# Kernel tuning notes

Measured on AMD Instinct MI355X. Metric: run time of the kernel, lower is better.

## Reference

```python
import jax, jax.numpy as jnp
import numpy as np

GROUPS = 8
EPS = 1e-3  # Keras GroupNormalization default epsilon


def group_norm(x, gamma, beta):
    b, h, w, c = x.shape
    xr = x.reshape(b, h, w, GROUPS, c // GROUPS)
    mean = jnp.mean(xr, axis=(1, 2, 4), keepdims=True)
    var = jnp.var(xr, axis=(1, 2, 4), keepdims=True)
    xn = ((xr - mean) * jax.lax.rsqrt(var + EPS)).reshape(b, h, w, c)
    return xn * gamma + beta


def setup_inputs() -> dict:
    key = jax.random.key(0)
    ks = jax.random.split(key, 6)
    B, H, W, C = 4, 64, 64, 256
    std = C ** -0.5
    return {
        "x": jax.random.normal(ks[0], (B, H, W, C), dtype=jnp.float32),
        "gamma": jnp.ones((C,), jnp.float32),
        "beta": jnp.zeros((C,), jnp.float32),
        "wq": jax.random.normal(ks[1], (C, C), jnp.float32) * std,
        "bq": jnp.zeros((C,), jnp.float32),
        "wk": jax.random.normal(ks[2], (C, C), jnp.float32) * std,
        "bk": jnp.zeros((C,), jnp.float32),
        "wv": jax.random.normal(ks[3], (C, C), jnp.float32) * std,
        "bv": jnp.zeros((C,), jnp.float32),
        "wp": jax.random.normal(ks[4], (C, C), jnp.float32) * std,
        "bp": jnp.zeros((C,), jnp.float32),
    }


def reference(x, gamma, beta, wq, bq, wk, bk, wv, bv, wp, bp):
    b, h, w, c = x.shape
    scale = jnp.asarray(c, x.dtype) ** -0.5
    xn = group_norm(x, gamma, beta)
    # 1x1 convs are per-pixel dense layers
    q = (xn @ wq + bq).reshape(b, h * w, c)
    k = (xn @ wk + bk).reshape(b, h * w, c)
    v = (xn @ wv + bv).reshape(b, h * w, c)
    scores = jnp.einsum('bic,bjc->bij', q, k) * scale  # [b, N, N]
    attn = jax.nn.softmax(scores, axis=-1)
    out = jnp.einsum('bij,bjc->bic', attn, v).reshape(b, h, w, c)
    return x + (out @ wp + bp)
```

## Files before the change

kernel.cpp:

```cpp
#include <hip/hip_runtime.h>

#define N_TOK 4096
#define C_DIM 256
#define BATCH 4
#define M_ROWS (BATCH * N_TOK)
#define GN_CNT 131072.0f
#define JSPLIT 4

typedef __attribute__((ext_vector_type(4))) float f32x4;
typedef __attribute__((ext_vector_type(16))) float f32x16;
typedef __attribute__((ext_vector_type(8))) short s16x8;
typedef __attribute__((ext_vector_type(4))) unsigned short u16x4;
typedef __attribute__((ext_vector_type(4))) unsigned int u32x4;

static __device__ __forceinline__ unsigned short f2bf(float f) {
  unsigned int u = __builtin_bit_cast(unsigned int, f);
  u += 0x7fff + ((u >> 16) & 1);
  return (unsigned short)(u >> 16);
}
static __device__ __forceinline__ float bf2f(unsigned short h) {
  unsigned int u = ((unsigned int)h) << 16;
  return __builtin_bit_cast(float, u);
}

static __device__ __forceinline__ void gload_lds16(const void* g, void* l) {
  __builtin_amdgcn_global_load_lds(
      (__attribute__((address_space(1))) void*)(unsigned long long)(const char*)g,
      (__attribute__((address_space(3))) void*)l, 16, 0, 0);
}

__global__ __launch_bounds__(256) void prep(const float* __restrict__ x,
                                            const float* __restrict__ wq,
                                            const float* __restrict__ wk,
                                            const float* __restrict__ wv,
                                            const float* __restrict__ wp,
                                            float* __restrict__ partials,
                                            unsigned short* __restrict__ wT) {
  int tid = threadIdx.x;
  if (blockIdx.x < 512) {
    int bg = blockIdx.x >> 4, chunk = blockIdx.x & 15;
    int b = bg >> 3, g = bg & 7;
    const f32x4* x4 = (const f32x4*)x;
    float s1 = 0.f, s2 = 0.f;
#pragma unroll
    for (int it = 0; it < 8; ++it) {
      int idx = it * 256 + tid;
      int nl = idx >> 3, cq = idx & 7;
      f32x4 v = x4[(b * N_TOK + chunk * 256 + nl) * 64 + g * 8 + cq];
      s1 += v[0] + v[1] + v[2] + v[3];
      s2 += v[0] * v[0] + v[1] * v[1] + v[2] * v[2] + v[3] * v[3];
    }
    for (int m = 1; m < 64; m <<= 1) {
      s1 += __shfl_xor(s1, m, 64);
      s2 += __shfl_xor(s2, m, 64);
    }
    __shared__ float r1[4], r2[4];
    int wave = tid >> 6, lane = tid & 63;
    if (lane == 0) { r1[wave] = s1; r2[wave] = s2; }
    __syncthreads();
    if (tid == 0) {
      int slot = (bg * 16 + chunk) * 2;
      partials[slot]     = r1[0] + r1[1] + r1[2] + r1[3];
      partials[slot + 1] = r2[0] + r2[1] + r2[2] + r2[3];
    }
  } else {
    int rem = blockIdx.x - 512;
    int z = rem >> 6, t = rem & 63;
    int k0 = (t >> 3) * 32, n0 = (t & 7) * 32;
    const float* const srcs[4] = {wq, wk, wv, wp};
    const float* w = srcs[z];
    unsigned short* o = wT + z * 65536;
    __shared__ float tt[32][33];
    int tx = tid & 31, ty = tid >> 5;
#pragma unroll
    for (int ky = 0; ky < 32; ky += 8)
      tt[ty + ky][tx] = w[(k0 + ty + ky) * C_DIM + n0 + tx];
    __syncthreads();
#pragma unroll
    for (int ky = 0; ky < 32; ky += 8)
      o[(n0 + ty + ky) * C_DIM + k0 + tx] = f2bf(tt[tx][ty + ky]);
  }
}

__global__ __launch_bounds__(256, 2) void qkv_gemm(const float* __restrict__ x,
                                                   const unsigned short* __restrict__ wT,
                                                   const float* __restrict__ partials,
                                                   const float* __restrict__ gamma,
                                                   const float* __restrict__ beta,
                                                   const float* __restrict__ bq,
                                                   const float* __restrict__ bk,
                                                   const float* __restrict__ bv,
                                                   unsigned short* __restrict__ qo,
                                                   unsigned short* __restrict__ ko,
                                                   unsigned short* __restrict__ vo) {
  int tid = threadIdx.x;
  int wave = tid >> 6, lane = tid & 63, n32 = lane & 31, half = lane >> 5;
  int row0 = blockIdx.x * 128 + wave * 32;
  int c0 = blockIdx.y * 128;
  int row = row0 + n32;
  int batch = blockIdx.x >> 5;
  __shared__ __align__(16) unsigned short Wt[32768];
  __shared__ float mean_s[8], rstd_s[8];

#pragma unroll
  for (int ii = 0; ii < 32; ++ii) {
    int u = ii * 256 + tid;
    int n = u >> 5, ku = u & 31;
    gload_lds16(wT + (size_t)(c0 + n) * C_DIM + ((ku ^ (n & 7)) * 8), Wt + u * 8);
  }
  if (tid < 8) {
    const float* p = partials + (batch * 8 + tid) * 32;
    float s1 = 0.f, s2 = 0.f;
#pragma unroll
    for (int c = 0; c < 16; ++c) { s1 += p[2 * c]; s2 += p[2 * c + 1]; }
    float inv = 1.f / GN_CNT;
    float m = s1 * inv, v = s2 * inv - m * m;
    mean_s[tid] = m;
    rstd_s[tid] = rsqrtf(v + 1e-3f);
  }
  __syncthreads();

  float mean[8], rstd[8];
#pragma unroll
  for (int g = 0; g < 8; ++g) { mean[g] = mean_s[g]; rstd[g] = rstd_s[g]; }
  s16x8 af[16];
#pragma unroll
  for (int ks = 0; ks < 16; ++ks) {
    int cb = ks * 16 + half * 8;
    const f32x4* xp = (const f32x4*)(x + (size_t)row * C_DIM + cb);
    f32x4 v0 = xp[0], v1 = xp[1];
    const f32x4* g4 = (const f32x4*)(gamma + cb);
    const f32x4* b4 = (const f32x4*)(beta + cb);
    f32x4 ga0 = g4[0], ga1 = g4[1], be0 = b4[0], be1 = b4[1];
    int g = (2 * ks + half) >> 2;
    float m = mean[g], rs = rstd[g];
    s16x8 o;
#pragma unroll
    for (int j = 0; j < 4; ++j) {
      o[j]     = (short)f2bf((v0[j] - m) * rs * ga0[j] + be0[j]);
      o[4 + j] = (short)f2bf((v1[j] - m) * rs * ga1[j] + be1[j]);
    }
    af[ks] = o;
  }

  for (int w = 0; w < 3; ++w) {
    if (w > 0) {
      __syncthreads();
#pragma unroll
      for (int ii = 0; ii < 32; ++ii) {
        int u = ii * 256 + tid;
        int n = u >> 5, ku = u & 31;
        gload_lds16(wT + (size_t)w * 65536 + (size_t)(c0 + n) * C_DIM + ((ku ^ (n & 7)) * 8),
                    Wt + u * 8);
      }
      __syncthreads();
    }
    const float* bias = (w == 0) ? bq : (w == 1) ? bk : bv;
    unsigned short* outp = (w == 0) ? qo : (w == 1) ? ko : vo;
    float scale = (w == 0) ? 0.0625f : 1.f;
#pragma unroll
    for (int ct = 0; ct < 4; ++ct) {
      int nl = ct * 32 + n32;
      f32x16 acc = (f32x16)(bias[c0 + nl]);
#pragma unroll
      for (int ks = 0; ks < 16; ++ks) {
        s16x8 wf = *(const s16x8*)(Wt + nl * C_DIM + (((2 * ks + half) ^ (nl & 7)) * 8));
        acc = __builtin_amdgcn_mfma_f32_32x32x16_bf16(af[ks], wf, acc, 0, 0, 0);
      }
#pragma unroll
      for (int r = 0; r < 16; ++r) {
        int rr = (r & 3) + 8 * (r >> 2) + 4 * half;
        outp[(size_t)(row0 + rr) * C_DIM + c0 + nl] = f2bf(acc[r] * scale);
      }
    }
  }
}

__global__ __launch_bounds__(256) void vtrans(const unsigned short* __restrict__ v,
                                              unsigned short* __restrict__ vT) {
  __shared__ unsigned short t[32][33];
  int n0 = blockIdx.x * 32, c0 = blockIdx.y * 32, b = blockIdx.z;
  int tx = threadIdx.x, ty = threadIdx.y;
#pragma unroll
  for (int ky = 0; ky < 32; ky += 8)
    t[ty + ky][tx] = v[(b * N_TOK + n0 + ty + ky) * C_DIM + c0 + tx];
  __syncthreads();
#pragma unroll
  for (int ky = 0; ky < 32; ky += 8)
    vT[(b * C_DIM + c0 + ty + ky) * N_TOK + n0 + tx] = t[tx][ty + ky];
}

__global__ __launch_bounds__(256, 2) void attn_part(const unsigned short* __restrict__ q,
                                                    const unsigned short* __restrict__ k,
                                                    const unsigned short* __restrict__ vT,
                                                    unsigned short* __restrict__ op0,
                                                    unsigned short* __restrict__ op1,
                                                    unsigned short* __restrict__ op2,
                                                    unsigned short* __restrict__ op3,
                                                    float* __restrict__ lbuf) {
  int tid = threadIdx.x;
  int wave = tid >> 6, lane = tid & 63;
  int n32 = lane & 31, half = lane >> 5;
  int i = blockIdx.x;
  int batch = (i >> 1) & 3;
  int slot = ((i >> 3) << 1) | (i & 1);
  int qb = slot & 31, chunk = slot >> 5;
  int qrow0 = batch * N_TOK + qb * 128 + wave * 32;
  const unsigned short* kb = k + (size_t)batch * N_TOK * C_DIM;
  const unsigned short* vb = vT + (size_t)batch * C_DIM * N_TOK;
  unsigned short* op = (chunk == 0) ? op0 : (chunk == 1) ? op1 : (chunk == 2) ? op2 : op3;

  __shared__ __align__(16) unsigned short Kt[2][8192];
  __shared__ __align__(16) unsigned short Vt[2][8192];

  const unsigned short* qp = q + (size_t)(qrow0 + n32) * C_DIM;
  s16x8 qf[16];
#pragma unroll
  for (int ks = 0; ks < 16; ++ks)
    qf[ks] = *(const s16x8*)(qp + ks * 16 + half * 8);

  f32x16 Oa[8];
#pragma unroll
  for (int ct = 0; ct < 8; ++ct) Oa[ct] = (f32x16)(0.f);
  float ls = 0.f;
  int swz = n32 & 7;

  {
    int jbase = chunk * 1024;
#pragma unroll
    for (int ii = 0; ii < 4; ++ii) {
      int u = ii * 256 + tid;
      int tok = u >> 5, un = u & 31;
      gload_lds16(kb + (size_t)(jbase + tok) * C_DIM + ((un ^ (tok & 7)) * 8), &Kt[0][u * 8]);
    }
#pragma unroll
    for (int ii = 0; ii < 4; ++ii) {
      gload_lds16(vb + (size_t)tid * N_TOK + jbase + ii * 8, &Vt[0][(ii * 256 + tid) * 8]);
    }
  }

  int cur = 0;
  for (int jt = 0; jt < 32; ++jt) {
    __syncthreads();
    if (jt < 31) {
      int jbase = chunk * 1024 + (jt + 1) * 32;
      int nxt = cur ^ 1;
#pragma unroll
      for (int ii = 0; ii < 4; ++ii) {
        int u = ii * 256 + tid;
        int tok = u >> 5, un = u & 31;
        gload_lds16(kb + (size_t)(jbase + tok) * C_DIM + ((un ^ (tok & 7)) * 8), &Kt[nxt][u * 8]);
      }
#pragma unroll
      for (int ii = 0; ii < 4; ++ii) {
        gload_lds16(vb + (size_t)tid * N_TOK + jbase + ii * 8, &Vt[nxt][(ii * 256 + tid) * 8]);
      }
    }
    const unsigned short* KT = Kt[cur];
    const unsigned short* VT = Vt[cur];

    f32x16 sc = (f32x16)(0.f);
#pragma unroll
    for (int ks = 0; ks < 16; ++ks) {
      s16x8 kf = *(const s16x8*)(KT + n32 * 256 + (((ks * 2 + half) ^ swz) * 8));
      sc = __builtin_amdgcn_mfma_f32_32x32x16_bf16(kf, qf[ks], sc, 0, 0, 0);
    }
    unsigned D[8];
#pragma unroll
    for (int t = 0; t < 8; ++t) {
      float pa = exp2f(fmaf(sc[2 * t],     1.44269504f, -11.54156032f));
      float pb = exp2f(fmaf(sc[2 * t + 1], 1.44269504f, -11.54156032f));
      ls += pa + pb;
      D[t] = (__builtin_bit_cast(unsigned, pa) >> 16) |
             (__builtin_bit_cast(unsigned, pb) & 0xFFFF0000u);
    }
    unsigned E[8];
#pragma unroll
    for (int t = 0; t < 8; ++t) E[t] = __shfl_xor(D[t], 32);
    u32x4 w0 = {half ? E[2] : D[0], half ? E[3] : D[1],
                half ? D[2] : E[0], half ? D[3] : E[1]};
    u32x4 w1 = {half ? E[6] : D[4], half ? E[7] : D[5],
                half ? D[6] : E[4], half ? D[7] : E[5]};
    s16x8 pf0 = __builtin_bit_cast(s16x8, w0);
    s16x8 pf1 = __builtin_bit_cast(s16x8, w1);
#pragma unroll
    for (int ct = 0; ct < 8; ++ct) {
      int ch = ct * 32 + n32;
      s16x8 vf0 = *(const s16x8*)(VT + (half * 256 + ch) * 8);
      s16x8 vf1 = *(const s16x8*)(VT + ((2 + half) * 256 + ch) * 8);
      Oa[ct] = __builtin_amdgcn_mfma_f32_32x32x16_bf16(pf0, vf0, Oa[ct], 0, 0, 0);
      Oa[ct] = __builtin_amdgcn_mfma_f32_32x32x16_bf16(pf1, vf1, Oa[ct], 0, 0, 0);
    }
    cur ^= 1;
  }
#pragma unroll
  for (int ct = 0; ct < 8; ++ct)
#pragma unroll
    for (int r = 0; r < 16; ++r) {
      int row = (r & 3) + 8 * (r >> 2) + 4 * half;
      op[(size_t)(qrow0 + row) * C_DIM + ct * 32 + n32] = f2bf(Oa[ct][r]);
    }
  float tot = ls + __shfl_xor(ls, 32);
  if (half == 0) lbuf[chunk * M_ROWS + qrow0 + n32] = tot;
}

__global__ __launch_bounds__(256, 2) void proj_gemm(const unsigned short* __restrict__ p0,
                                                    const unsigned short* __restrict__ p1,
                                                    const unsigned short* __restrict__ p2,
                                                    const unsigned short* __restrict__ p3,
                                                    const float* __restrict__ lbuf,
                                                    const unsigned short* __restrict__ wt,
                                                    const float* __restrict__ bp,
                                                    const float* __restrict__ x,
                                                    float* __restrict__ out) {
  int tid = threadIdx.x;
  int wave = tid >> 6, lane = tid & 63, n32 = lane & 31, half = lane >> 5;
  int row0 = blockIdx.x * 128 + wave * 32;
  int c0 = blockIdx.y * 128;
  __shared__ __align__(16) unsigned short Wt[32768];

#pragma unroll
  for (int ii = 0; ii < 32; ++ii) {
    int u = ii * 256 + tid;
    int n = u >> 5, ku = u & 31;
    gload_lds16(wt + (size_t)(c0 + n) * C_DIM + ((ku ^ (n & 7)) * 8), Wt + u * 8);
  }

  int row = row0 + n32;
  float linv = 1.f / (lbuf[row] + lbuf[M_ROWS + row] +
                      lbuf[2 * M_ROWS + row] + lbuf[3 * M_ROWS + row]);
  s16x8 af[16];
#pragma unroll
  for (int ks = 0; ks < 16; ++ks) {
    size_t off = (size_t)row * C_DIM + ks * 16 + half * 8;
    s16x8 a0 = *(const s16x8*)(p0 + off);
    s16x8 a1 = *(const s16x8*)(p1 + off);
    s16x8 a2 = *(const s16x8*)(p2 + off);
    s16x8 a3 = *(const s16x8*)(p3 + off);
    s16x8 o;
#pragma unroll
    for (int j = 0; j < 8; ++j) {
      float f = bf2f((unsigned short)a0[j]) + bf2f((unsigned short)a1[j]) +
                bf2f((unsigned short)a2[j]) + bf2f((unsigned short)a3[j]);
      o[j] = (short)f2bf(f * linv);
    }
    af[ks] = o;
  }
  __syncthreads();

#pragma unroll
  for (int ct = 0; ct < 4; ++ct) {
    int nl = ct * 32 + n32;
    f32x16 acc = (f32x16)(bp[c0 + nl]);
#pragma unroll
    for (int ks = 0; ks < 16; ++ks) {
      s16x8 wf = *(const s16x8*)(Wt + nl * C_DIM + (((2 * ks + half) ^ (nl & 7)) * 8));
      acc = __builtin_amdgcn_mfma_f32_32x32x16_bf16(af[ks], wf, acc, 0, 0, 0);
    }
#pragma unroll
    for (int r = 0; r < 16; ++r) {
      int rr = (r & 3) + 8 * (r >> 2) + 4 * half;
      size_t idx = (size_t)(row0 + rr) * C_DIM + c0 + nl;
      out[idx] = acc[r] + x[idx];
    }
  }
}

extern "C" void kernel_launch(void* const* d_in, const int* in_sizes, int n_in,
                              void* d_out, int out_size, void* d_ws, size_t ws_size,
                              hipStream_t stream) {
  const float* x     = (const float*)d_in[0];
  const float* gamma = (const float*)d_in[1];
  const float* beta  = (const float*)d_in[2];
  const float* wq    = (const float*)d_in[3];
  const float* bq    = (const float*)d_in[4];
  const float* wk    = (const float*)d_in[5];
  const float* bk    = (const float*)d_in[6];
  const float* wv    = (const float*)d_in[7];
  const float* bv    = (const float*)d_in[8];
  const float* wp    = (const float*)d_in[9];
  const float* bp    = (const float*)d_in[10];
  float* out = (float*)d_out;

  char* ws = (char*)d_ws;
  const size_t MC = (size_t)M_ROWS * C_DIM;
  float* partials      = (float*)ws;
  unsigned short* wT   = (unsigned short*)(ws + 4096);
  unsigned short* qb   = wT + 4 * 65536;
  unsigned short* kbuf = qb + MC;
  unsigned short* vb   = kbuf + MC;
  unsigned short* vTb  = vb + MC;
  unsigned short* pl0  = vTb + MC;
  unsigned short* pl2  = pl0 + MC;
  unsigned short* pl3  = pl2 + MC;
  float* lbuf          = (float*)(pl3 + MC);
  unsigned short* pl1  = vb;

  prep<<<768, 256, 0, stream>>>(x, wq, wk, wv, wp, partials, wT);
  qkv_gemm<<<dim3(128, 2), 256, 0, stream>>>(x, wT, partials, gamma, beta,
                                             bq, bk, bv, qb, kbuf, vb);
  vtrans<<<dim3(128, 8, 4), dim3(32, 8), 0, stream>>>(vb, vTb);
  attn_part<<<512, 256, 0, stream>>>(qb, kbuf, vTb, pl0, pl1, pl2, pl3, lbuf);
  proj_gemm<<<dim3(128, 2), 256, 0, stream>>>(pl0, pl1, pl2, pl3, lbuf,
                                              wT + 3 * 65536, bp, x, out);
}
```

Before: 219.5 us.

## Read K directly from global in attention, halve GEMM column tiles, add setprio

The attention kernel no longer stages K tiles in LDS with double buffering. Each lane now loads K fragments straight from global memory, which relies on cache hits and frees LDS space. The P·V MFMA loop is wrapped in s_setprio raises so waves doing matrix work get scheduling priority. The QKV and projection GEMMs use 64-column tiles with twice as many blocks and a launch bound of 3, which cuts LDS per block to allow more occupancy but repeats the A-operand normalisation and loads per column tile.

```diff
diff --git a/kernel.cpp b/kernel.cpp
--- a/kernel.cpp
+++ b/kernel.cpp
@@ -5,7 +5,6 @@
 #define BATCH 4
 #define M_ROWS (BATCH * N_TOK)
 #define GN_CNT 131072.0f
-#define JSPLIT 4
 
 typedef __attribute__((ext_vector_type(4))) float f32x4;
 typedef __attribute__((ext_vector_type(16))) float f32x16;
@@ -82,7 +81,7 @@
   }
 }
 
-__global__ __launch_bounds__(256, 2) void qkv_gemm(const float* __restrict__ x,
+__global__ __launch_bounds__(256, 3) void qkv_gemm(const float* __restrict__ x,
                                                    const unsigned short* __restrict__ wT,
                                                    const float* __restrict__ partials,
                                                    const float* __restrict__ gamma,
@@ -96,14 +95,14 @@
   int tid = threadIdx.x;
   int wave = tid >> 6, lane = tid & 63, n32 = lane & 31, half = lane >> 5;
   int row0 = blockIdx.x * 128 + wave * 32;
-  int c0 = blockIdx.y * 128;
+  int c0 = blockIdx.y * 64;
   int row = row0 + n32;
   int batch = blockIdx.x >> 5;
-  __shared__ __align__(16) unsigned short Wt[32768];
+  __shared__ __align__(16) unsigned short Wt[16384];
   __shared__ float mean_s[8], rstd_s[8];
 
 #pragma unroll
-  for (int ii = 0; ii < 32; ++ii) {
+  for (int ii = 0; ii < 8; ++ii) {
     int u = ii * 256 + tid;
     int n = u >> 5, ku = u & 31;
     gload_lds16(wT + (size_t)(c0 + n) * C_DIM + ((ku ^ (n & 7)) * 8), Wt + u * 8);
@@ -147,7 +146,7 @@
     if (w > 0) {
       __syncthreads();
 #pragma unroll
-      for (int ii = 0; ii < 32; ++ii) {
+      for (int ii = 0; ii < 8; ++ii) {
         int u = ii * 256 + tid;
         int n = u >> 5, ku = u & 31;
         gload_lds16(wT + (size_t)w * 65536 + (size_t)(c0 + n) * C_DIM + ((ku ^ (n & 7)) * 8),
@@ -159,7 +158,7 @@
     unsigned short* outp = (w == 0) ? qo : (w == 1) ? ko : vo;
     float scale = (w == 0) ? 0.0625f : 1.f;
 #pragma unroll
-    for (int ct = 0; ct < 4; ++ct) {
+    for (int ct = 0; ct < 2; ++ct) {
       int nl = ct * 32 + n32;
       f32x16 acc = (f32x16)(bias[c0 + nl]);
 #pragma unroll
@@ -210,7 +209,6 @@
   const unsigned short* vb = vT + (size_t)batch * C_DIM * N_TOK;
   unsigned short* op = (chunk == 0) ? op0 : (chunk == 1) ? op1 : (chunk == 2) ? op2 : op3;
 
-  __shared__ __align__(16) unsigned short Kt[2][8192];
   __shared__ __align__(16) unsigned short Vt[2][8192];
 
   const unsigned short* qp = q + (size_t)(qrow0 + n32) * C_DIM;
@@ -223,46 +221,27 @@
 #pragma unroll
   for (int ct = 0; ct < 8; ++ct) Oa[ct] = (f32x16)(0.f);
   float ls = 0.f;
-  int swz = n32 & 7;
-
-  {
-    int jbase = chunk * 1024;
-#pragma unroll
-    for (int ii = 0; ii < 4; ++ii) {
-      int u = ii * 256 + tid;
-      int tok = u >> 5, un = u & 31;
-      gload_lds16(kb + (size_t)(jbase + tok) * C_DIM + ((un ^ (tok & 7)) * 8), &Kt[0][u * 8]);
-    }
-#pragma unroll
-    for (int ii = 0; ii < 4; ++ii) {
-      gload_lds16(vb + (size_t)tid * N_TOK + jbase + ii * 8, &Vt[0][(ii * 256 + tid) * 8]);
-    }
-  }
+
+  int jbase0 = chunk * 1024;
+#pragma unroll
+  for (int ii = 0; ii < 4; ++ii)
+    gload_lds16(vb + (size_t)tid * N_TOK + jbase0 + ii * 8, &Vt[0][(ii * 256 + tid) * 8]);
 
   int cur = 0;
   for (int jt = 0; jt < 32; ++jt) {
     __syncthreads();
     if (jt < 31) {
-      int jbase = chunk * 1024 + (jt + 1) * 32;
+      int jb2 = jbase0 + (jt + 1) * 32;
       int nxt = cur ^ 1;
 #pragma unroll
-      for (int ii = 0; ii < 4; ++ii) {
-        int u = ii * 256 + tid;
-        int tok = u >> 5, un = u & 31;
-        gload_lds16(kb + (size_t)(jbase + tok) * C_DIM + ((un ^ (tok & 7)) * 8), &Kt[nxt][u * 8]);
-      }
-#pragma unroll
-      for (int ii = 0; ii < 4; ++ii) {
-        gload_lds16(vb + (size_t)tid * N_TOK + jbase + ii * 8, &Vt[nxt][(ii * 256 + tid) * 8]);
-      }
-    }
-    const unsigned short* KT = Kt[cur];
-    const unsigned short* VT = Vt[cur];
-
+      for (int ii = 0; ii < 4; ++ii)
+        gload_lds16(vb + (size_t)tid * N_TOK + jb2 + ii * 8, &Vt[nxt][(ii * 256 + tid) * 8]);
+    }
+    const unsigned short* kp = kb + (size_t)(jbase0 + jt * 32 + n32) * C_DIM;
     f32x16 sc = (f32x16)(0.f);
 #pragma unroll
     for (int ks = 0; ks < 16; ++ks) {
-      s16x8 kf = *(const s16x8*)(KT + n32 * 256 + (((ks * 2 + half) ^ swz) * 8));
+      s16x8 kf = *(const s16x8*)(kp + ks * 16 + half * 8);
       sc = __builtin_amdgcn_mfma_f32_32x32x16_bf16(kf, qf[ks], sc, 0, 0, 0);
     }
     unsigned D[8];
@@ -283,6 +262,8 @@
                 half ? D[6] : E[4], half ? D[7] : E[5]};
     s16x8 pf0 = __builtin_bit_cast(s16x8, w0);
     s16x8 pf1 = __builtin_bit_cast(s16x8, w1);
+    const unsigned short* VT = Vt[cur];
+    __builtin_amdgcn_s_setprio(1);
 #pragma unroll
     for (int ct = 0; ct < 8; ++ct) {
       int ch = ct * 32 + n32;
@@ -291,6 +272,7 @@
       Oa[ct] = __builtin_amdgcn_mfma_f32_32x32x16_bf16(pf0, vf0, Oa[ct], 0, 0, 0);
       Oa[ct] = __builtin_amdgcn_mfma_f32_32x32x16_bf16(pf1, vf1, Oa[ct], 0, 0, 0);
     }
+    __builtin_amdgcn_s_setprio(0);
     cur ^= 1;
   }
 #pragma unroll
@@ -304,7 +286,7 @@
   if (half == 0) lbuf[chunk * M_ROWS + qrow0 + n32] = tot;
 }
 
-__global__ __launch_bounds__(256, 2) void proj_gemm(const unsigned short* __restrict__ p0,
+__global__ __launch_bounds__(256, 3) void proj_gemm(const unsigned short* __restrict__ p0,
                                                     const unsigned short* __restrict__ p1,
                                                     const unsigned short* __restrict__ p2,
                                                     const unsigned short* __restrict__ p3,
@@ -316,11 +298,11 @@
   int tid = threadIdx.x;
   int wave = tid >> 6, lane = tid & 63, n32 = lane & 31, half = lane >> 5;
   int row0 = blockIdx.x * 128 + wave * 32;
-  int c0 = blockIdx.y * 128;
-  __shared__ __align__(16) unsigned short Wt[32768];
-
-#pragma unroll
-  for (int ii = 0; ii < 32; ++ii) {
+  int c0 = blockIdx.y * 64;
+  __shared__ __align__(16) unsigned short Wt[16384];
+
+#pragma unroll
+  for (int ii = 0; ii < 8; ++ii) {
     int u = ii * 256 + tid;
     int n = u >> 5, ku = u & 31;
     gload_lds16(wt + (size_t)(c0 + n) * C_DIM + ((ku ^ (n & 7)) * 8), Wt + u * 8);
@@ -349,7 +331,7 @@
   __syncthreads();
 
 #pragma unroll
-  for (int ct = 0; ct < 4; ++ct) {
+  for (int ct = 0; ct < 2; ++ct) {
     int nl = ct * 32 + n32;
     f32x16 acc = (f32x16)(bp[c0 + nl]);
 #pragma unroll
@@ -397,10 +379,10 @@
   unsigned short* pl1  = vb;
 
   prep<<<768, 256, 0, stream>>>(x, wq, wk, wv, wp, partials, wT);
-  qkv_gemm<<<dim3(128, 2), 256, 0, stream>>>(x, wT, partials, gamma, beta,
+  qkv_gemm<<<dim3(128, 4), 256, 0, stream>>>(x, wT, partials, gamma, beta,
                                              bq, bk, bv, qb, kbuf, vb);
   vtrans<<<dim3(128, 8, 4), dim3(32, 8), 0, stream>>>(vb, vTb);
   attn_part<<<512, 256, 0, stream>>>(qb, kbuf, vTb, pl0, pl1, pl2, pl3, lbuf);
-  proj_gemm<<<dim3(128, 2), 256, 0, stream>>>(pl0, pl1, pl2, pl3, lbuf,
+  proj_gemm<<<dim3(128, 4), 256, 0, stream>>>(pl0, pl1, pl2, pl3, lbuf,
                                               wT + 3 * 65536, bp, x, out);
 }
```

Result: slower. 328.7 us (+49.7%).
